# Optimization experiments

Measured on AMD Instinct MI355X. Metric: run time of the kernel, lower is better.

The kernel has to match this reference:

```python
import jax, jax.numpy as jnp
import numpy as np

B, T, DIM = 2, 2048, 2048
H, HKV = 32, 8
HD = DIM // H            # 64
NREP = H // HKV          # 4
ROPE_BASE = 10000.0


def setup_inputs() -> dict:
    key = jax.random.key(0)
    kx, kq, kk, kv, ko = jax.random.split(key, 5)
    s = 1.0 / np.sqrt(DIM)
    x = jax.random.normal(kx, (B, T, DIM), dtype=jnp.float32)
    wq = jax.random.normal(kq, (DIM, H * HD), dtype=jnp.float32) * s
    wk = jax.random.normal(kk, (DIM, HKV * HD), dtype=jnp.float32) * s
    wv = jax.random.normal(kv, (DIM, HKV * HD), dtype=jnp.float32) * s
    wo = jax.random.normal(ko, (H * HD, DIM), dtype=jnp.float32) * s
    # freqs_cis = exp(i * t * theta_j), theta_j = base^{-2j/head_dim}
    theta = ROPE_BASE ** (-np.arange(0, HD, 2, dtype=np.float32) / HD)  # [HD/2]
    ang = np.arange(T, dtype=np.float32)[:, None] * theta[None, :]      # [T, HD/2]
    freqs_cos = jnp.asarray(np.cos(ang), dtype=jnp.float32)
    freqs_sin = jnp.asarray(np.sin(ang), dtype=jnp.float32)
    return {"x": x, "freqs_cos": freqs_cos, "freqs_sin": freqs_sin,
            "wq": wq, "wk": wk, "wv": wv, "wo": wo}


def _rope(x, cos, sin):
    # x: [B, h, T, HD]; cos/sin: [T, HD/2]. Complex mult on (even, odd) pairs.
    xr = x[..., 0::2]
    xi = x[..., 1::2]
    c = cos[None, None, :, :]
    s = sin[None, None, :, :]
    out_r = xr * c - xi * s
    out_i = xr * s + xi * c
    return jnp.stack([out_r, out_i], axis=-1).reshape(x.shape)


def reference(x, freqs_cos, freqs_sin, wq, wk, wv, wo):
    Bx, Tx, _ = x.shape
    q = (x @ wq).reshape(Bx, Tx, H, HD).transpose(0, 2, 1, 3)      # [B,H,T,HD]
    k = (x @ wk).reshape(Bx, Tx, HKV, HD).transpose(0, 2, 1, 3)    # [B,HKV,T,HD]
    v = (x @ wv).reshape(Bx, Tx, HKV, HD).transpose(0, 2, 1, 3)
    q = _rope(q, freqs_cos[:Tx], freqs_sin[:Tx])
    k = _rope(k, freqs_cos[:Tx], freqs_sin[:Tx])
    # GQA: group query heads per kv head instead of repeat_interleave of K/V.
    qg = q.reshape(Bx, HKV, NREP, Tx, HD)
    scale = 1.0 / jnp.sqrt(jnp.asarray(HD, dtype=x.dtype))
    scores = jnp.einsum('bgrqd,bgkd->bgrqk', qg, k) * scale        # [B,HKV,NREP,T,T]
    causal = jnp.tril(jnp.ones((Tx, Tx), dtype=bool))
    scores = jnp.where(causal[None, None, None], scores, jnp.asarray(-jnp.inf, scores.dtype))
    p = jax.nn.softmax(scores.astype(jnp.float32), axis=-1).astype(x.dtype)
    out = jnp.einsum('bgrqk,bgkd->bgrqd', p, v)                    # [B,HKV,NREP,T,HD]
    out = out.reshape(Bx, H, Tx, HD).transpose(0, 2, 1, 3).reshape(Bx, Tx, H * HD)
    return out @ wo
```

## Files before the change

kernel.cpp:

```cpp
#include <hip/hip_runtime.h>
#include <cstdint>
#include <cstddef>

#define B_    2
#define T_    2048
#define DIM_  2048
#define H_    32
#define HKV_  8
#define HD_   64
#define NQKV  3072

typedef __attribute__((ext_vector_type(8))) __bf16 bf16x8;
typedef __attribute__((ext_vector_type(4))) float  f32x4;

typedef __attribute__((address_space(1))) void GV;
typedef __attribute__((address_space(3))) void LV;

__device__ __forceinline__ void gload_lds16(const void* g, void* l) {
  __builtin_amdgcn_global_load_lds((const GV*)g, (LV*)l, 16, 0, 0);
}

__device__ __forceinline__ unsigned short f2bf(float f) {
  union { float f; unsigned int u; } c;
  c.f = f;
  unsigned int r = (c.u + 0x7FFFu + ((c.u >> 16) & 1u)) >> 16;
  return (unsigned short)r;
}

__device__ __forceinline__ unsigned int cvt_pk_bf16(float lo, float hi) {
  unsigned int r;
  asm("v_cvt_pk_bf16_f32 %0, %1, %2" : "=v"(r) : "v"(lo), "v"(hi));
  return r;
}

__global__ __launch_bounds__(256) void k_transpose_w(const float* __restrict__ in,
                                                     unsigned short* __restrict__ out,
                                                     int R, int C) {
  __shared__ float tile[32][33];
  int c0 = blockIdx.x * 32, r0 = blockIdx.y * 32;
  int tx = threadIdx.x, ty = threadIdx.y;
#pragma unroll
  for (int i = 0; i < 32; i += 8)
    tile[ty + i][tx] = in[(size_t)(r0 + ty + i) * C + c0 + tx];
  __syncthreads();
#pragma unroll
  for (int i = 0; i < 32; i += 8)
    out[(size_t)(c0 + ty + i) * R + r0 + tx] = f2bf(tile[tx][ty + i]);
}

__global__ __launch_bounds__(256) void k_cvt_bf16(const float* __restrict__ in,
                                                  unsigned short* __restrict__ out, int n4) {
  int i = blockIdx.x * blockDim.x + threadIdx.x;
  if (i >= n4) return;
  float4 v = reinterpret_cast<const float4*>(in)[i];
  ushort4 o;
  o.x = f2bf(v.x); o.y = f2bf(v.y); o.z = f2bf(v.z); o.w = f2bf(v.w);
  reinterpret_cast<ushort4*>(out)[i] = o;
}

__global__ __launch_bounds__(256, 2) void k_gemm_bt(const unsigned short* __restrict__ A,
                                                    const unsigned short* __restrict__ Bm,
                                                    float* __restrict__ C,
                                                    int M, int N, int K) {
  __shared__ unsigned short Asl[128 * 32];
  __shared__ unsigned short Bsl[128 * 32];
  const int m0 = blockIdx.y * 128, n0 = blockIdx.x * 128;
  const int tid = threadIdx.x;
  const int l = tid & 63, wid = tid >> 6;
  const int wr = wid >> 1, wc = wid & 1;
  const int lc = l & 15, lr = l >> 4;
  const int srow = tid >> 2;
  const int sc8 = (tid & 3) * 8;
  const unsigned short* Ag = A + (size_t)m0 * K;
  const unsigned short* Bg = Bm + (size_t)n0 * K;

  f32x4 acc[4][4] = {};

  for (int k0 = 0; k0 < K; k0 += 32) {
    __syncthreads();
    gload_lds16(Ag + (size_t)srow * K + k0 + sc8,        &Asl[srow * 32 + sc8]);
    gload_lds16(Ag + (size_t)(srow + 64) * K + k0 + sc8, &Asl[(srow + 64) * 32 + sc8]);
    gload_lds16(Bg + (size_t)srow * K + k0 + sc8,        &Bsl[srow * 32 + sc8]);
    gload_lds16(Bg + (size_t)(srow + 64) * K + k0 + sc8, &Bsl[(srow + 64) * 32 + sc8]);
    __syncthreads();
    bf16x8 af[4], bfr[4];
#pragma unroll
    for (int mi = 0; mi < 4; ++mi)
      af[mi] = *(const bf16x8*)&Asl[(wr * 64 + mi * 16 + lc) * 32 + lr * 8];
#pragma unroll
    for (int ni = 0; ni < 4; ++ni)
      bfr[ni] = *(const bf16x8*)&Bsl[(wc * 64 + ni * 16 + lc) * 32 + lr * 8];
#pragma unroll
    for (int mi = 0; mi < 4; ++mi)
#pragma unroll
      for (int ni = 0; ni < 4; ++ni)
        acc[mi][ni] = __builtin_amdgcn_mfma_f32_16x16x32_bf16(af[mi], bfr[ni], acc[mi][ni], 0, 0, 0);
  }

#pragma unroll
  for (int mi = 0; mi < 4; ++mi)
#pragma unroll
    for (int ni = 0; ni < 4; ++ni) {
      int row = m0 + wr * 64 + mi * 16 + lr * 4;
      int col = n0 + wc * 64 + ni * 16 + lc;
      float* Cp = C + (size_t)row * N + col;
#pragma unroll
      for (int rr = 0; rr < 4; ++rr) Cp[(size_t)rr * N] = acc[mi][ni][rr];
    }
}

__global__ __launch_bounds__(256) void k_rope_q(const float* __restrict__ qkv,
                                                const float* __restrict__ fc,
                                                const float* __restrict__ fs,
                                                unsigned short* __restrict__ qb) {
  int tid = blockIdx.x * 256 + threadIdx.x;
  int i = tid & 31;
  int h = (tid >> 5) & 31;
  int bt = tid >> 10;
  int b = bt >> 11, t = bt & 2047;
  float2 x = reinterpret_cast<const float2*>(qkv + (size_t)bt * NQKV + h * 64)[i];
  float c = fc[t * 32 + i], s = fs[t * 32 + i];
  ushort2 o;
  o.x = f2bf(x.x * c - x.y * s);
  o.y = f2bf(x.x * s + x.y * c);
  reinterpret_cast<ushort2*>(qb + ((size_t)(b * H_ + h) * T_ + t) * HD_)[i] = o;
}

__global__ __launch_bounds__(256) void k_rope_k(const float* __restrict__ qkv,
                                                const float* __restrict__ fc,
                                                const float* __restrict__ fs,
                                                unsigned short* __restrict__ kb) {
  int tid = blockIdx.x * 256 + threadIdx.x;
  int i = tid & 31;
  int hk = (tid >> 5) & 7;
  int bt = tid >> 8;
  int b = bt >> 11, t = bt & 2047;
  float2 x = reinterpret_cast<const float2*>(qkv + (size_t)bt * NQKV + 2048 + hk * 64)[i];
  float c = fc[t * 32 + i], s = fs[t * 32 + i];
  ushort2 o;
  o.x = f2bf(x.x * c - x.y * s);
  o.y = f2bf(x.x * s + x.y * c);
  reinterpret_cast<ushort2*>(kb + ((size_t)(b * HKV_ + hk) * T_ + t) * HD_)[i] = o;
}

__global__ __launch_bounds__(256) void k_vtrans(const float* __restrict__ qkv,
                                                unsigned short* __restrict__ vt) {
  __shared__ unsigned short tile[64][65];
  int t0 = blockIdx.x * 64;
  int bh = blockIdx.y;
  int tx = threadIdx.x, ty = threadIdx.y;
  int b = bh >> 3, hk = bh & 7;
  int colbase = 2560 + hk * 64;
#pragma unroll
  for (int tt = 0; tt < 16; ++tt) {
    int tr = tt * 4 + ty;
    tile[tr][tx] = f2bf(qkv[(size_t)(b * T_ + t0 + tr) * NQKV + colbase + tx]);
  }
  __syncthreads();
  size_t obase = (size_t)bh * 64 * T_;
#pragma unroll
  for (int tt = 0; tt < 16; ++tt) {
    int d = tt * 4 + ty;
    vt[obase + (size_t)d * T_ + t0 + tx] = tile[tx][d];
  }
}

__global__ __launch_bounds__(256, 2) void k_flash(const unsigned short* __restrict__ Q,
                                                  const unsigned short* __restrict__ Kt,
                                                  const unsigned short* __restrict__ Vt,
                                                  unsigned short* __restrict__ O) {
  const int qb = (int)(gridDim.x - 1 - blockIdx.x);
  const int h = blockIdx.y, b = blockIdx.z;
  const int hk = h >> 2;
  const int tid = threadIdx.x, w = tid >> 6, l = tid & 63;
  const int lr = l >> 4, lc = l & 15;

  const size_t qbase = (size_t)(b * H_ + h) * T_ * HD_;
  const size_t kbase = (size_t)(b * HKV_ + hk) * T_ * HD_;
  const size_t vbase = (size_t)(b * HKV_ + hk) * HD_ * T_;
  const int q0 = qb * 128;
  const int wrow = q0 + w * 32;

  bf16x8 qf[2][2];
#pragma unroll
  for (int f = 0; f < 2; ++f)
#pragma unroll
    for (int ks = 0; ks < 2; ++ks)
      qf[f][ks] = *(const bf16x8*)&Q[qbase + (size_t)(wrow + f * 16 + lc) * HD_ + ks * 32 + lr * 8];

  f32x4 o[2][4] = {};
  float m[2] = {-1e30f, -1e30f}, lsum[2] = {0.f, 0.f};

  const int nt = qb * 2 + 1 + (w >> 1);
  const float SC = 0.125f * 1.44269504f;
  const int srcA = lc + 32 * (lr & 1);

  for (int kvt = 0; kvt < nt; ++kvt) {
    const int kv0 = kvt * 64;

    bf16x8 kf[2][4];
#pragma unroll
    for (int ks = 0; ks < 2; ++ks)
#pragma unroll
      for (int ni = 0; ni < 4; ++ni)
        kf[ks][ni] = *(const bf16x8*)&Kt[kbase + (size_t)(kv0 + ni * 16 + lc) * HD_ + ks * 32 + lr * 8];

    f32x4 s0[4] = {}, s1[4] = {};
    __builtin_amdgcn_s_setprio(1);
#pragma unroll
    for (int ks = 0; ks < 2; ++ks)
#pragma unroll
      for (int ni = 0; ni < 4; ++ni) {
        s0[ni] = __builtin_amdgcn_mfma_f32_16x16x32_bf16(kf[ks][ni], qf[0][ks], s0[ni], 0, 0, 0);
        s1[ni] = __builtin_amdgcn_mfma_f32_16x16x32_bf16(kf[ks][ni], qf[1][ks], s1[ni], 0, 0, 0);
      }
    __builtin_amdgcn_s_setprio(0);

    bf16x8 vf[2][4];
#pragma unroll
    for (int ks = 0; ks < 2; ++ks)
#pragma unroll
      for (int di = 0; di < 4; ++di)
        vf[ks][di] = *(const bf16x8*)&Vt[vbase + (size_t)(di * 16 + lc) * T_ + kv0 + ks * 32 + lr * 8];

    bf16x8 pa[2][2];

#pragma unroll
    for (int f = 0; f < 2; ++f) {
      f32x4* s = (f == 0) ? s0 : s1;
      const int qrow_f = wrow + f * 16;
      const bool domask = (kv0 + 63 > qrow_f);

      float pm = -1e30f;
#pragma unroll
      for (int ni = 0; ni < 4; ++ni)
#pragma unroll
        for (int r = 0; r < 4; ++r) {
          float sv = s[ni][r] * SC;
          if (domask && (kv0 + ni * 16 + lr * 4 + r > qrow_f + lc)) sv = -1e30f;
          s[ni][r] = sv;
          pm = fmaxf(pm, sv);
        }
      pm = fmaxf(pm, __shfl_xor(pm, 16));
      pm = fmaxf(pm, __shfl_xor(pm, 32));

      if (!__all(pm <= m[f] + 8.f)) {
        float mn = fmaxf(m[f], pm);
        float al = __builtin_amdgcn_exp2f(m[f] - mn);
        m[f] = mn;
        lsum[f] *= al;
        float av0 = __shfl(al, lr * 4 + 0);
        float av1 = __shfl(al, lr * 4 + 1);
        float av2 = __shfl(al, lr * 4 + 2);
        float av3 = __shfl(al, lr * 4 + 3);
#pragma unroll
        for (int di = 0; di < 4; ++di) {
          o[f][di][0] *= av0; o[f][di][1] *= av1;
          o[f][di][2] *= av2; o[f][di][3] *= av3;
        }
      }

      float ps = 0.f;
      unsigned int P01[4], P23[4];
#pragma unroll
      for (int ni = 0; ni < 4; ++ni) {
        float p0 = __builtin_amdgcn_exp2f(s[ni][0] - m[f]);
        float p1 = __builtin_amdgcn_exp2f(s[ni][1] - m[f]);
        float p2 = __builtin_amdgcn_exp2f(s[ni][2] - m[f]);
        float p3 = __builtin_amdgcn_exp2f(s[ni][3] - m[f]);
        ps += (p0 + p1) + (p2 + p3);
        P01[ni] = cvt_pk_bf16(p0, p1);
        P23[ni] = cvt_pk_bf16(p2, p3);
      }
      ps += __shfl_xor(ps, 16);
      ps += __shfl_xor(ps, 32);
      lsum[f] += ps;

#pragma unroll
      for (int ks = 0; ks < 2; ++ks) {
        unsigned int a0 = __shfl(P01[2 * ks], srcA);
        unsigned int a1 = __shfl(P23[2 * ks], srcA);
        unsigned int a2 = __shfl(P01[2 * ks], srcA + 16);
        unsigned int a3 = __shfl(P23[2 * ks], srcA + 16);
        unsigned int b0 = __shfl(P01[2 * ks + 1], srcA);
        unsigned int b1 = __shfl(P23[2 * ks + 1], srcA);
        unsigned int b2 = __shfl(P01[2 * ks + 1], srcA + 16);
        unsigned int b3 = __shfl(P23[2 * ks + 1], srcA + 16);
        const bool hi = (lr >= 2);
        union { unsigned int u[4]; bf16x8 v; } pw;
        pw.u[0] = hi ? b0 : a0;
        pw.u[1] = hi ? b1 : a1;
        pw.u[2] = hi ? b2 : a2;
        pw.u[3] = hi ? b3 : a3;
        pa[f][ks] = pw.v;
      }
    }

    __builtin_amdgcn_s_setprio(1);
#pragma unroll
    for (int ks = 0; ks < 2; ++ks)
#pragma unroll
      for (int di = 0; di < 4; ++di) {
        o[0][di] = __builtin_amdgcn_mfma_f32_16x16x32_bf16(pa[0][ks], vf[ks][di], o[0][di], 0, 0, 0);
        o[1][di] = __builtin_amdgcn_mfma_f32_16x16x32_bf16(pa[1][ks], vf[ks][di], o[1][di], 0, 0, 0);
      }
    __builtin_amdgcn_s_setprio(0);
  }

#pragma unroll
  for (int f = 0; f < 2; ++f) {
    float i0 = 1.f / __shfl(lsum[f], lr * 4 + 0);
    float i1 = 1.f / __shfl(lsum[f], lr * 4 + 1);
    float i2 = 1.f / __shfl(lsum[f], lr * 4 + 2);
    float i3 = 1.f / __shfl(lsum[f], lr * 4 + 3);
#pragma unroll
    for (int di = 0; di < 4; ++di) {
      int row = wrow + f * 16 + lr * 4;
      size_t base = (size_t)(b * T_ + row) * DIM_ + h * 64 + di * 16 + lc;
      O[base]             = f2bf(o[f][di][0] * i0);
      O[base + DIM_]      = f2bf(o[f][di][1] * i1);
      O[base + 2 * DIM_]  = f2bf(o[f][di][2] * i2);
      O[base + 3 * DIM_]  = f2bf(o[f][di][3] * i3);
    }
  }
}

extern "C" void kernel_launch(void* const* d_in, const int* in_sizes, int n_in,
                              void* d_out, int out_size, void* d_ws, size_t ws_size,
                              hipStream_t stream) {
  const float* x  = (const float*)d_in[0];
  const float* fc = (const float*)d_in[1];
  const float* fs = (const float*)d_in[2];
  const float* wq = (const float*)d_in[3];
  const float* wk = (const float*)d_in[4];
  const float* wv = (const float*)d_in[5];
  const float* wo = (const float*)d_in[6];
  float* out = (float*)d_out;
  char* ws = (char*)d_ws;

  unsigned short* xb   = (unsigned short*)(ws);
  unsigned short* wT   = (unsigned short*)(ws + 16777216);
  unsigned short* woT  = (unsigned short*)(ws + 29360128);
  float*          qkv  = (float*)(ws + 37748736);
  unsigned short* qb   = (unsigned short*)(ws + 88080384);
  unsigned short* kb   = (unsigned short*)(ws + 104857600);
  unsigned short* vt   = (unsigned short*)(ws + 109051904);
  unsigned short* attn = (unsigned short*)(ws + 37748736);

  dim3 tb(32, 8);
  k_transpose_w<<<dim3(64, 64), tb, 0, stream>>>(wq, wT, 2048, 2048);
  k_transpose_w<<<dim3(16, 64), tb, 0, stream>>>(wk, wT + (size_t)2048 * 2048, 2048, 512);
  k_transpose_w<<<dim3(16, 64), tb, 0, stream>>>(wv, wT + (size_t)2560 * 2048, 2048, 512);
  k_transpose_w<<<dim3(64, 64), tb, 0, stream>>>(wo, woT, 2048, 2048);
  k_cvt_bf16<<<8192, 256, 0, stream>>>(x, xb, 2097152);

  k_gemm_bt<<<dim3(NQKV / 128, 4096 / 128), 256, 0, stream>>>(xb, wT, qkv, 4096, NQKV, 2048);

  k_rope_q<<<16384, 256, 0, stream>>>(qkv, fc, fs, qb);
  k_rope_k<<<4096, 256, 0, stream>>>(qkv, fc, fs, kb);
  k_vtrans<<<dim3(T_ / 64, B_ * HKV_), dim3(64, 4), 0, stream>>>(qkv, vt);

  k_flash<<<dim3(T_ / 128, H_, B_), 256, 0, stream>>>(qb, kb, vt, attn);

  k_gemm_bt<<<dim3(2048 / 128, 4096 / 128), 256, 0, stream>>>(attn, woT, out, 4096, 2048, 2048);
}
```

Baseline: 487.2 us.

## Pair causal query tiles per block for balanced flash-attention work and K prefetch

```diff
diff --git a/kernel.cpp b/kernel.cpp
--- a/kernel.cpp
+++ b/kernel.cpp
@@ -169,113 +169,96 @@
                                                   const unsigned short* __restrict__ Kt,
                                                   const unsigned short* __restrict__ Vt,
                                                   unsigned short* __restrict__ O) {
-  const int qb = (int)(gridDim.x - 1 - blockIdx.x);
-  const int h = blockIdx.y, b = blockIdx.z;
-  const int hk = h >> 2;
+  const int bid = blockIdx.x;
+  const int hk = bid & 7;
+  const int slot = bid >> 3;
+  const int pq = slot & 15;
+  const int hrem = slot >> 4;
+  const int h = hk * 4 + hrem;
+
   const int tid = threadIdx.x, w = tid >> 6, l = tid & 63;
   const int lr = l >> 4, lc = l & 15;
-
-  const size_t qbase = (size_t)(b * H_ + h) * T_ * HD_;
-  const size_t kbase = (size_t)(b * HKV_ + hk) * T_ * HD_;
-  const size_t vbase = (size_t)(b * HKV_ + hk) * HD_ * T_;
-  const int q0 = qb * 128;
-  const int wrow = q0 + w * 32;
-
-  bf16x8 qf[2][2];
-#pragma unroll
-  for (int f = 0; f < 2; ++f)
-#pragma unroll
-    for (int ks = 0; ks < 2; ++ks)
-      qf[f][ks] = *(const bf16x8*)&Q[qbase + (size_t)(wrow + f * 16 + lc) * HD_ + ks * 32 + lr * 8];
-
-  f32x4 o[2][4] = {};
-  float m[2] = {-1e30f, -1e30f}, lsum[2] = {0.f, 0.f};
-
-  const int nt = qb * 2 + 1 + (w >> 1);
   const float SC = 0.125f * 1.44269504f;
   const int srcA = lc + 32 * (lr & 1);
-
-  for (int kvt = 0; kvt < nt; ++kvt) {
-    const int kv0 = kvt * 64;
-
-    bf16x8 kf[2][4];
-#pragma unroll
-    for (int ks = 0; ks < 2; ++ks)
-#pragma unroll
-      for (int ni = 0; ni < 4; ++ni)
-        kf[ks][ni] = *(const bf16x8*)&Kt[kbase + (size_t)(kv0 + ni * 16 + lc) * HD_ + ks * 32 + lr * 8];
-
-    f32x4 s0[4] = {}, s1[4] = {};
-    __builtin_amdgcn_s_setprio(1);
-#pragma unroll
-    for (int ks = 0; ks < 2; ++ks)
-#pragma unroll
-      for (int ni = 0; ni < 4; ++ni) {
-        s0[ni] = __builtin_amdgcn_mfma_f32_16x16x32_bf16(kf[ks][ni], qf[0][ks], s0[ni], 0, 0, 0);
-        s1[ni] = __builtin_amdgcn_mfma_f32_16x16x32_bf16(kf[ks][ni], qf[1][ks], s1[ni], 0, 0, 0);
-      }
-    __builtin_amdgcn_s_setprio(0);
-
-    bf16x8 vf[2][4];
-#pragma unroll
-    for (int ks = 0; ks < 2; ++ks)
-#pragma unroll
-      for (int di = 0; di < 4; ++di)
-        vf[ks][di] = *(const bf16x8*)&Vt[vbase + (size_t)(di * 16 + lc) * T_ + kv0 + ks * 32 + lr * 8];
-
-    bf16x8 pa[2][2];
-
-#pragma unroll
-    for (int f = 0; f < 2; ++f) {
-      f32x4* s = (f == 0) ? s0 : s1;
-      const int qrow_f = wrow + f * 16;
-      const bool domask = (kv0 + 63 > qrow_f);
-
-      float pm = -1e30f;
-#pragma unroll
-      for (int ni = 0; ni < 4; ++ni)
-#pragma unroll
-        for (int r = 0; r < 4; ++r) {
-          float sv = s[ni][r] * SC;
-          if (domask && (kv0 + ni * 16 + lr * 4 + r > qrow_f + lc)) sv = -1e30f;
-          s[ni][r] = sv;
-          pm = fmaxf(pm, sv);
-        }
+  const bool hi = (lr >= 2);
+
+  for (int tsk = 0; tsk < 2; ++tsk) {
+    const int b = tsk;
+    const int p = tsk ? (15 - pq) : pq;
+    const int qlo = p, qhi = 31 - p;
+
+    const size_t qbase = (size_t)(b * H_ + h) * T_ * HD_;
+    const size_t kbase = (size_t)(b * HKV_ + hk) * T_ * HD_;
+    const size_t vbase = (size_t)(b * HKV_ + hk) * HD_ * T_;
+    const int rowL = qlo * 64 + w * 16;
+    const int rowH = qhi * 64 + w * 16;
+
+    bf16x8 qL[2], qH[2];
+#pragma unroll
+    for (int ks = 0; ks < 2; ++ks) {
+      qL[ks] = *(const bf16x8*)&Q[qbase + (size_t)(rowL + lc) * HD_ + ks * 32 + lr * 8];
+      qH[ks] = *(const bf16x8*)&Q[qbase + (size_t)(rowH + lc) * HD_ + ks * 32 + lr * 8];
+    }
+
+    f32x4 oL[4] = {}, oH[4] = {};
+    float mL = -1e30f, mH = -1e30f, lsL = 0.f, lsH = 0.f;
+
+    auto loadK = [&](bf16x8 (&kf)[2][4], int kv0x) {
+#pragma unroll
+      for (int ks = 0; ks < 2; ++ks)
+#pragma unroll
+        for (int ni = 0; ni < 4; ++ni)
+          kf[ks][ni] = *(const bf16x8*)&Kt[kbase + (size_t)(kv0x + ni * 16 + lc) * HD_ + ks * 32 + lr * 8];
+    };
+
+    auto softmax = [&](f32x4 (&s)[4], int kv0, int qrow0, bool diag,
+                       float& m, float& ls, f32x4 (&o)[4], bf16x8 (&pa)[2]) {
+      if (diag) {
+        const int qcol = qrow0 + lc;
+#pragma unroll
+        for (int ni = 0; ni < 4; ++ni)
+#pragma unroll
+          for (int r = 0; r < 4; ++r)
+            if (kv0 + ni * 16 + lr * 4 + r > qcol) s[ni][r] = -1e30f;
+      }
+      float x0 = fmaxf(fmaxf(s[0][0], s[0][1]), fmaxf(s[0][2], s[0][3]));
+      float x1 = fmaxf(fmaxf(s[1][0], s[1][1]), fmaxf(s[1][2], s[1][3]));
+      float x2 = fmaxf(fmaxf(s[2][0], s[2][1]), fmaxf(s[2][2], s[2][3]));
+      float x3 = fmaxf(fmaxf(s[3][0], s[3][1]), fmaxf(s[3][2], s[3][3]));
+      float pm = fmaxf(fmaxf(x0, x1), fmaxf(x2, x3));
       pm = fmaxf(pm, __shfl_xor(pm, 16));
       pm = fmaxf(pm, __shfl_xor(pm, 32));
-
-      if (!__all(pm <= m[f] + 8.f)) {
-        float mn = fmaxf(m[f], pm);
-        float al = __builtin_amdgcn_exp2f(m[f] - mn);
-        m[f] = mn;
-        lsum[f] *= al;
+      const float pms = pm * SC;
+      if (!__all(pms <= m + 8.f)) {
+        float mn = fmaxf(m, pms);
+        float al = __builtin_amdgcn_exp2f(m - mn);
+        m = mn;
+        ls *= al;
         float av0 = __shfl(al, lr * 4 + 0);
         float av1 = __shfl(al, lr * 4 + 1);
         float av2 = __shfl(al, lr * 4 + 2);
         float av3 = __shfl(al, lr * 4 + 3);
 #pragma unroll
         for (int di = 0; di < 4; ++di) {
-          o[f][di][0] *= av0; o[f][di][1] *= av1;
-          o[f][di][2] *= av2; o[f][di][3] *= av3;
+          o[di][0] *= av0; o[di][1] *= av1;
+          o[di][2] *= av2; o[di][3] *= av3;
         }
       }
-
       float ps = 0.f;
       unsigned int P01[4], P23[4];
 #pragma unroll
       for (int ni = 0; ni < 4; ++ni) {
-        float p0 = __builtin_amdgcn_exp2f(s[ni][0] - m[f]);
-        float p1 = __builtin_amdgcn_exp2f(s[ni][1] - m[f]);
-        float p2 = __builtin_amdgcn_exp2f(s[ni][2] - m[f]);
-        float p3 = __builtin_amdgcn_exp2f(s[ni][3] - m[f]);
+        float p0 = __builtin_amdgcn_exp2f(__builtin_fmaf(s[ni][0], SC, -m));
+        float p1 = __builtin_amdgcn_exp2f(__builtin_fmaf(s[ni][1], SC, -m));
+        float p2 = __builtin_amdgcn_exp2f(__builtin_fmaf(s[ni][2], SC, -m));
+        float p3 = __builtin_amdgcn_exp2f(__builtin_fmaf(s[ni][3], SC, -m));
         ps += (p0 + p1) + (p2 + p3);
         P01[ni] = cvt_pk_bf16(p0, p1);
         P23[ni] = cvt_pk_bf16(p2, p3);
       }
       ps += __shfl_xor(ps, 16);
       ps += __shfl_xor(ps, 32);
-      lsum[f] += ps;
-
+      ls += ps;
 #pragma unroll
       for (int ks = 0; ks < 2; ++ks) {
         unsigned int a0 = __shfl(P01[2 * ks], srcA);
@@ -286,42 +269,89 @@
         unsigned int b1 = __shfl(P23[2 * ks + 1], srcA);
         unsigned int b2 = __shfl(P01[2 * ks + 1], srcA + 16);
         unsigned int b3 = __shfl(P23[2 * ks + 1], srcA + 16);
-        const bool hi = (lr >= 2);
         union { unsigned int u[4]; bf16x8 v; } pw;
         pw.u[0] = hi ? b0 : a0;
         pw.u[1] = hi ? b1 : a1;
         pw.u[2] = hi ? b2 : a2;
         pw.u[3] = hi ? b3 : a3;
-        pa[f][ks] = pw.v;
-      }
+        pa[ks] = pw.v;
+      }
+    };
+
+    bf16x8 kf[2][4];
+    loadK(kf, 0);
+
+    for (int kvt = 0; kvt <= qhi; ++kvt) {
+      const int kv0 = kvt * 64;
+      const bool doL = (kvt <= qlo);
+
+      bf16x8 vf[2][4];
+#pragma unroll
+      for (int ks = 0; ks < 2; ++ks)
+#pragma unroll
+        for (int di = 0; di < 4; ++di)
+          vf[ks][di] = *(const bf16x8*)&Vt[vbase + (size_t)(di * 16 + lc) * T_ + kv0 + ks * 32 + lr * 8];
+
+      f32x4 s[4] = {};
+      __builtin_amdgcn_s_setprio(1);
+#pragma unroll
+      for (int ks = 0; ks < 2; ++ks)
+#pragma unroll
+        for (int ni = 0; ni < 4; ++ni)
+          s[ni] = __builtin_amdgcn_mfma_f32_16x16x32_bf16(kf[ks][ni], qH[ks], s[ni], 0, 0, 0);
+      __builtin_amdgcn_s_setprio(0);
+
+      bf16x8 paH[2], paL[2];
+      softmax(s, kv0, rowH, kvt == qhi, mH, lsH, oH, paH);
+
+      if (doL) {
+        f32x4 s2[4] = {};
+        __builtin_amdgcn_s_setprio(1);
+#pragma unroll
+        for (int ks = 0; ks < 2; ++ks)
+#pragma unroll
+          for (int ni = 0; ni < 4; ++ni)
+            s2[ni] = __builtin_amdgcn_mfma_f32_16x16x32_bf16(kf[ks][ni], qL[ks], s2[ni], 0, 0, 0);
+        __builtin_amdgcn_s_setprio(0);
+        if (kvt < qhi) loadK(kf, kv0 + 64);
+        softmax(s2, kv0, rowL, kvt == qlo, mL, lsL, oL, paL);
+      } else {
+        if (kvt < qhi) loadK(kf, kv0 + 64);
+      }
+
+      __builtin_amdgcn_s_setprio(1);
+#pragma unroll
+      for (int ks = 0; ks < 2; ++ks)
+#pragma unroll
+        for (int di = 0; di < 4; ++di)
+          oH[di] = __builtin_amdgcn_mfma_f32_16x16x32_bf16(paH[ks], vf[ks][di], oH[di], 0, 0, 0);
+      if (doL) {
+#pragma unroll
+        for (int ks = 0; ks < 2; ++ks)
+#pragma unroll
+          for (int di = 0; di < 4; ++di)
+            oL[di] = __builtin_amdgcn_mfma_f32_16x16x32_bf16(paL[ks], vf[ks][di], oL[di], 0, 0, 0);
+      }
+      __builtin_amdgcn_s_setprio(0);
     }
 
-    __builtin_amdgcn_s_setprio(1);
-#pragma unroll
-    for (int ks = 0; ks < 2; ++ks)
+    auto epi = [&](f32x4 (&o)[4], float ls, int row0) {
+      float i0 = 1.f / __shfl(ls, lr * 4 + 0);
+      float i1 = 1.f / __shfl(ls, lr * 4 + 1);
+      float i2 = 1.f / __shfl(ls, lr * 4 + 2);
+      float i3 = 1.f / __shfl(ls, lr * 4 + 3);
 #pragma unroll
       for (int di = 0; di < 4; ++di) {
-        o[0][di] = __builtin_amdgcn_mfma_f32_16x16x32_bf16(pa[0][ks], vf[ks][di], o[0][di], 0, 0, 0);
-        o[1][di] = __builtin_amdgcn_mfma_f32_16x16x32_bf16(pa[1][ks], vf[ks][di], o[1][di], 0, 0, 0);
-      }
-    __builtin_amdgcn_s_setprio(0);
-  }
-
-#pragma unroll
-  for (int f = 0; f < 2; ++f) {
-    float i0 = 1.f / __shfl(lsum[f], lr * 4 + 0);
-    float i1 = 1.f / __shfl(lsum[f], lr * 4 + 1);
-    float i2 = 1.f / __shfl(lsum[f], lr * 4 + 2);
-    float i3 = 1.f / __shfl(lsum[f], lr * 4 + 3);
-#pragma unroll
-    for (int di = 0; di < 4; ++di) {
-      int row = wrow + f * 16 + lr * 4;
-      size_t base = (size_t)(b * T_ + row) * DIM_ + h * 64 + di * 16 + lc;
-      O[base]             = f2bf(o[f][di][0] * i0);
-      O[base + DIM_]      = f2bf(o[f][di][1] * i1);
-      O[base + 2 * DIM_]  = f2bf(o[f][di][2] * i2);
-      O[base + 3 * DIM_]  = f2bf(o[f][di][3] * i3);
-    }
+        int row = row0 + lr * 4;
+        size_t base = (size_t)(b * T_ + row) * DIM_ + h * 64 + di * 16 + lc;
+        O[base]            = f2bf(o[di][0] * i0);
+        O[base + DIM_]     = f2bf(o[di][1] * i1);
+        O[base + 2 * DIM_] = f2bf(o[di][2] * i2);
+        O[base + 3 * DIM_] = f2bf(o[di][3] * i3);
+      }
+    };
+    epi(oH, lsH, rowH);
+    epi(oL, lsL, rowL);
   }
 }
 
@@ -360,7 +390,7 @@
   k_rope_k<<<4096, 256, 0, stream>>>(qkv, fc, fs, kb);
   k_vtrans<<<dim3(T_ / 64, B_ * HKV_), dim3(64, 4), 0, stream>>>(qkv, vt);
 
-  k_flash<<<dim3(T_ / 128, H_, B_), 256, 0, stream>>>(qb, kb, vt, attn);
+  k_flash<<<512, 256, 0, stream>>>(qb, kb, vt, attn);
 
   k_gemm_bt<<<dim3(2048 / 128, 4096 / 128), 256, 0, stream>>>(attn, woT, out, 4096, 2048, 2048);
 }
```

New measurement: 435.9 us. 10.5% less time.
